# Kernel optimization log

Hardware: AMD Instinct MI355X
Metric: run time of the kernel (lower is better)

The kernel has to match this reference:

```python
import jax, jax.numpy as jnp
import numpy as np

E, NB, F, H = 30, 12, 1024, 32  # numEmotions, numBasicEmotions, numCommonFeatures, hidden
EPS = 1e-12  # F.normalize eps


def setup_inputs() -> dict:
    key = jax.random.key(0)
    ks = jax.random.split(key, 7)
    B, L = 8192, 128
    return {
        "basicEmotionDistributions": jax.random.uniform(ks[0], (B, NB, L), dtype=jnp.float32),
        "encodedFeatures": jax.random.normal(ks[1], (B, F), dtype=jnp.float32),
        "allBasicEmotionWeights": jax.random.normal(ks[2], (E, 1, NB, 1), dtype=jnp.float32),
        "W1": jax.random.normal(ks[3], (E, F, H), dtype=jnp.float32) / np.sqrt(F),
        "b1": jax.random.normal(ks[4], (E, H), dtype=jnp.float32) * 0.01,
        "W2": jax.random.normal(ks[5], (E, H, NB), dtype=jnp.float32) / np.sqrt(H),
        "b2": jax.random.normal(ks[6], (E, NB), dtype=jnp.float32) * 0.01,
    }


def reference(basicEmotionDistributions, encodedFeatures, allBasicEmotionWeights, W1, b1, W2, b2):
    # L1-normalize exp(weights) along basic-emotion dim: (E, NB)
    ew = jnp.exp(allBasicEmotionWeights[:, 0, :, 0])  # (E, NB)
    allW = ew / jnp.maximum(jnp.sum(jnp.abs(ew), axis=1, keepdims=True), EPS)

    # Batched per-emotion 2-layer MLP: (E, B, NB)
    h = jax.nn.selu(jnp.einsum('bf,efh->ebh', encodedFeatures, W1) + b1[:, None, :])
    mlp = jnp.einsum('ebh,ehn->ebn', h, W2) + b2[:, None, :]

    # updated weights and signed L1 normalization over NB dim
    updated = allW[:, None, :] + mlp  # (E, B, NB)
    # sign(x) * normalize(|x|, p=1) == x / max(sum|x|, eps)
    w = updated / jnp.maximum(jnp.sum(jnp.abs(updated), axis=2, keepdims=True), EPS)

    # weighted sum over basic emotions, then softmax over emotion length
    mixed = jnp.einsum('ebn,bnl->ebl', w, basicEmotionDistributions)  # (E, B, L)
    return jax.nn.softmax(mixed, axis=2)
```

## Files before the change

kernel.cpp:

```cpp
#include <hip/hip_runtime.h>

typedef __attribute__((ext_vector_type(8))) _Float16 half8;
typedef __attribute__((ext_vector_type(4))) float f32x4;

#define GAS(p) ((const __attribute__((address_space(1))) void*)(p))
#define LAS(p) ((__attribute__((address_space(3))) void*)(p))

__global__ __launch_bounds__(256) void cvt_pre(const float* __restrict__ feat,
                                               const float* __restrict__ W1,
                                               _Float16* __restrict__ A16,
                                               _Float16* __restrict__ W1T) {
    if (blockIdx.x < 4096) {
        int gid = blockIdx.x * 256 + threadIdx.x;
        int k8   = gid & 3;
        int m    = (gid >> 2) & 15;
        int frag = gid >> 6;
        int mf = frag & 7;
        int kc = (frag >> 3) & 31;
        int bt = frag >> 8;
        int b  = bt * 128 + mf * 16 + m;
        int f0 = kc * 32 + k8 * 8;
        const float4* src = (const float4*)(feat + (size_t)b * 1024 + f0);
        float4 v0 = src[0], v1 = src[1];
        half8 o;
        o[0] = (_Float16)v0.x; o[1] = (_Float16)v0.y;
        o[2] = (_Float16)v0.z; o[3] = (_Float16)v0.w;
        o[4] = (_Float16)v1.x; o[5] = (_Float16)v1.y;
        o[6] = (_Float16)v1.z; o[7] = (_Float16)v1.w;
        *(half8*)(A16 + ((size_t)frag * 64 + k8 * 16 + m) * 8) = o;
    } else {
        int gid = (blockIdx.x - 4096) * 256 + threadIdx.x;
        int k8   = gid & 3;
        int n    = (gid >> 2) & 15;
        int frag = gid >> 6;
        int nf = frag & 1;
        int kc = (frag >> 1) & 31;
        int e  = frag >> 6;
        int h  = nf * 16 + n;
        int f0 = kc * 32 + k8 * 8;
        const float* src = W1 + ((size_t)e * 1024 + f0) * 32 + h;
        half8 o;
#pragma unroll
        for (int j = 0; j < 8; ++j) o[j] = (_Float16)src[j * 32];
        *(half8*)(W1T + ((size_t)frag * 64 + k8 * 16 + n) * 8) = o;
    }
}

__global__ __launch_bounds__(256) void gemm_mlp(
    const _Float16* __restrict__ A16, const _Float16* __restrict__ W1T,
    const float* __restrict__ b1, const float* __restrict__ W2,
    const float* __restrict__ b2, const float* __restrict__ wts,
    float* __restrict__ wbuf) {
    __shared__ __align__(16) unsigned char smem[28672];
    unsigned char* Ash = smem;
    unsigned char* Bsh = smem + 16384;
    float* w2s = (float*)(smem + 24576);
    float* cb2 = (float*)(smem + 27648);
    float* ews = cb2 + 24;
    float* h_sh = (float*)smem;

    const int tid = threadIdx.x;
    const int e0 = blockIdx.x * 2;
    const int bt = blockIdx.y;
    const int w  = tid >> 6, l = tid & 63;
    const int q  = l >> 4, lc = l & 15;

    for (int i = tid; i < 768; i += 256) w2s[i] = W2[e0 * 384 + i];
    if (tid < 24) {
        cb2[tid] = b2[e0 * 12 + tid];
        ews[tid] = __expf(wts[e0 * 12 + tid]);
    }

    const _Float16* Abase = A16 + (size_t)bt * 131072;
    const _Float16* Bbase = W1T + (size_t)e0 * 32768;

    f32x4 zero = {0.f, 0.f, 0.f, 0.f};
    f32x4 acc[2][4];
#pragma unroll
    for (int i = 0; i < 2; ++i)
#pragma unroll
        for (int j = 0; j < 4; ++j) acc[i][j] = zero;

    for (int it = 0; it < 16; ++it) {
        const _Float16* Ait = Abase + it * 8192;
#pragma unroll
        for (int i = 0; i < 4; ++i) {
            int s = w * 4 + i;
            __builtin_amdgcn_global_load_lds(GAS(Ait + s * 512 + l * 8),
                                             LAS(Ash + s * 1024), 16, 0, 0);
        }
#pragma unroll
        for (int j = 0; j < 2; ++j) {
            int f  = w * 2 + j;
            int be = f >> 2, kn = f & 3;
            __builtin_amdgcn_global_load_lds(
                GAS(Bbase + be * 32768 + it * 2048 + kn * 512 + l * 8),
                LAS(Bsh + f * 1024), 16, 0, 0);
        }
        __syncthreads();
#pragma unroll
        for (int kc2 = 0; kc2 < 2; ++kc2) {
            half8 a0  = *(half8*)(Ash + (kc2 * 8 + 2 * w + 0) * 1024 + l * 16);
            half8 a1  = *(half8*)(Ash + (kc2 * 8 + 2 * w + 1) * 1024 + l * 16);
            half8 b00 = *(half8*)(Bsh + (0 + kc2 * 2 + 0) * 1024 + l * 16);
            half8 b01 = *(half8*)(Bsh + (0 + kc2 * 2 + 1) * 1024 + l * 16);
            half8 b10 = *(half8*)(Bsh + (4 + kc2 * 2 + 0) * 1024 + l * 16);
            half8 b11 = *(half8*)(Bsh + (4 + kc2 * 2 + 1) * 1024 + l * 16);
            acc[0][0] = __builtin_amdgcn_mfma_f32_16x16x32_f16(a0, b00, acc[0][0], 0, 0, 0);
            acc[0][1] = __builtin_amdgcn_mfma_f32_16x16x32_f16(a0, b01, acc[0][1], 0, 0, 0);
            acc[0][2] = __builtin_amdgcn_mfma_f32_16x16x32_f16(a0, b10, acc[0][2], 0, 0, 0);
            acc[0][3] = __builtin_amdgcn_mfma_f32_16x16x32_f16(a0, b11, acc[0][3], 0, 0, 0);
            acc[1][0] = __builtin_amdgcn_mfma_f32_16x16x32_f16(a1, b00, acc[1][0], 0, 0, 0);
            acc[1][1] = __builtin_amdgcn_mfma_f32_16x16x32_f16(a1, b01, acc[1][1], 0, 0, 0);
            acc[1][2] = __builtin_amdgcn_mfma_f32_16x16x32_f16(a1, b10, acc[1][2], 0, 0, 0);
            acc[1][3] = __builtin_amdgcn_mfma_f32_16x16x32_f16(a1, b11, acc[1][3], 0, 0, 0);
        }
        __syncthreads();
    }

    const float SC = 1.0507009873554805f, AL = 1.6732632423543772f;
    const int m2 = tid >> 1, sub = tid & 1;

#pragma unroll
    for (int eo = 0; eo < 2; ++eo) {
        const float b1a = b1[(e0 + eo) * 32 + lc];
        const float b1b = b1[(e0 + eo) * 32 + 16 + lc];
#pragma unroll
        for (int mf = 0; mf < 2; ++mf)
#pragma unroll
            for (int nf = 0; nf < 2; ++nf)
#pragma unroll
                for (int r = 0; r < 4; ++r) {
                    int m   = w * 32 + mf * 16 + q * 4 + r;
                    int col = nf * 16 + lc;
                    float x = acc[mf][eo * 2 + nf][r] + (nf ? b1b : b1a);
                    float hv = x > 0.f ? SC * x : SC * AL * (__expf(x) - 1.f);
                    h_sh[m * 33 + col] = hv;
                }
        __syncthreads();

        float u[6] = {0.f, 0.f, 0.f, 0.f, 0.f, 0.f};
        const float* hrow = h_sh + m2 * 33;
        const float* wbase = w2s + eo * 384 + sub * 6;
#pragma unroll 8
        for (int h = 0; h < 32; ++h) {
            float hv = hrow[h];
            const float* wr = wbase + h * 12;
#pragma unroll
            for (int j = 0; j < 6; ++j) u[j] += hv * wr[j];
        }
        float sew = 0.f;
#pragma unroll
        for (int i = 0; i < 12; ++i) sew += ews[eo * 12 + i];
        sew = fmaxf(sew, 1e-12f);
        float sabs = 0.f;
#pragma unroll
        for (int j = 0; j < 6; ++j) {
            u[j] += cb2[eo * 12 + sub * 6 + j] + ews[eo * 12 + sub * 6 + j] / sew;
            sabs += fabsf(u[j]);
        }
        sabs += __shfl_xor(sabs, 1);
        float inv = 1.f / fmaxf(sabs, 1e-12f);
        int b = bt * 128 + m2;
        float* dst = wbuf + (size_t)(e0 + eo) * 98304 + b * 12 + sub * 6;
#pragma unroll
        for (int j = 0; j < 6; ++j) dst[j] = u[j] * inv;
        __syncthreads();
    }
}

__global__ __launch_bounds__(256) void mix_softmax(
    const float* __restrict__ dist, const float* __restrict__ wbuf,
    float* __restrict__ out) {
    __shared__ float wsm[8 * 360];
    const int tid = threadIdx.x;
    const int b0 = blockIdx.x * 8;
    for (int i = tid; i < 2880; i += 256) {
        int e = i / 96, r = i - e * 96;
        wsm[(r / 12) * 360 + e * 12 + (r % 12)] = wbuf[(size_t)e * 98304 + b0 * 12 + r];
    }
    __syncthreads();
    const int m = tid >> 5, l4 = tid & 31;
    const int b = b0 + m;
    const float* dbase = dist + (size_t)b * 1536 + l4 * 4;
    f32x4 d[12];
#pragma unroll
    for (int n = 0; n < 12; ++n) d[n] = *(const f32x4*)(dbase + n * 128);
    const float* wrow = wsm + m * 360;
    for (int e = 0; e < 30; ++e) {
        const float* wr = wrow + e * 12;
        f32x4 a = {0.f, 0.f, 0.f, 0.f};
#pragma unroll
        for (int n = 0; n < 12; ++n) a += wr[n] * d[n];
        f32x4 ex;
        ex[0] = __expf(a[0]); ex[1] = __expf(a[1]);
        ex[2] = __expf(a[2]); ex[3] = __expf(a[3]);
        float sm = ex[0] + ex[1] + ex[2] + ex[3];
#pragma unroll
        for (int s = 16; s >= 1; s >>= 1) sm += __shfl_xor(sm, s);
        f32x4 o = ex * (1.f / sm);
        *(f32x4*)(out + ((size_t)e * 8192 + b) * 128 + l4 * 4) = o;
    }
}

extern "C" void kernel_launch(void* const* d_in, const int* in_sizes, int n_in,
                              void* d_out, int out_size, void* d_ws, size_t ws_size,
                              hipStream_t stream) {
    const float* dist = (const float*)d_in[0];
    const float* feat = (const float*)d_in[1];
    const float* wts  = (const float*)d_in[2];
    const float* W1   = (const float*)d_in[3];
    const float* b1   = (const float*)d_in[4];
    const float* W2   = (const float*)d_in[5];
    const float* b2   = (const float*)d_in[6];
    float* out = (float*)d_out;

    _Float16* A16 = (_Float16*)d_ws;
    _Float16* W1T = (_Float16*)((char*)d_ws + 16777216);
    float*   wbuf = (float*)((char*)d_ws + 16777216 + 1966080);

    cvt_pre<<<4576, 256, 0, stream>>>(feat, W1, A16, W1T);
    dim3 g1(15, 64);
    gemm_mlp<<<g1, 256, 0, stream>>>(A16, W1T, b1, W2, b2, wts, wbuf);
    mix_softmax<<<1024, 256, 0, stream>>>(dist, wbuf, out);
}
```

Baseline: 251.3 us.

## Process three emotions per GEMM block with swizzled 1D grid and repacked W2

```diff
diff --git a/kernel.cpp b/kernel.cpp
--- a/kernel.cpp
+++ b/kernel.cpp
@@ -51,22 +51,29 @@
     const float* __restrict__ b1, const float* __restrict__ W2,
     const float* __restrict__ b2, const float* __restrict__ wts,
     float* __restrict__ wbuf) {
-    __shared__ __align__(16) unsigned char smem[28672];
+    __shared__ __align__(16) unsigned char smem[33600];
     unsigned char* Ash = smem;
     unsigned char* Bsh = smem + 16384;
-    float* w2s = (float*)(smem + 24576);
-    float* cb2 = (float*)(smem + 27648);
-    float* ews = cb2 + 24;
+    float* w2s = (float*)(smem + 28672);
+    float* cb2 = (float*)(smem + 33280);
+    float* ews = cb2 + 36;
     float* h_sh = (float*)smem;
 
     const int tid = threadIdx.x;
-    const int e0 = blockIdx.x * 2;
-    const int bt = blockIdx.y;
+    const int bid = blockIdx.x;
+    const int v   = bid >> 3;
+    const int bt  = ((bid & 7) << 3) | (v & 7);
+    const int e0  = (v >> 3) * 3;
     const int w  = tid >> 6, l = tid & 63;
     const int q  = l >> 4, lc = l & 15;
 
-    for (int i = tid; i < 768; i += 256) w2s[i] = W2[e0 * 384 + i];
-    if (tid < 24) {
+    for (int i = tid; i < 1152; i += 256) {
+        int eo = i / 384, rr = i - eo * 384;
+        int h  = rr / 12, n = rr - h * 12;
+        int sb = n / 6,  j = n - sb * 6;
+        w2s[eo * 384 + sb * 192 + h * 6 + j] = W2[e0 * 384 + i];
+    }
+    if (tid < 36) {
         cb2[tid] = b2[e0 * 12 + tid];
         ews[tid] = __expf(wts[e0 * 12 + tid]);
     }
@@ -75,11 +82,11 @@
     const _Float16* Bbase = W1T + (size_t)e0 * 32768;
 
     f32x4 zero = {0.f, 0.f, 0.f, 0.f};
-    f32x4 acc[2][4];
+    f32x4 acc[2][6];
 #pragma unroll
     for (int i = 0; i < 2; ++i)
 #pragma unroll
-        for (int j = 0; j < 4; ++j) acc[i][j] = zero;
+        for (int j = 0; j < 6; ++j) acc[i][j] = zero;
 
     for (int it = 0; it < 16; ++it) {
         const _Float16* Ait = Abase + it * 8192;
@@ -90,8 +97,8 @@
                                              LAS(Ash + s * 1024), 16, 0, 0);
         }
 #pragma unroll
-        for (int j = 0; j < 2; ++j) {
-            int f  = w * 2 + j;
+        for (int j = 0; j < 3; ++j) {
+            int f  = w * 3 + j;
             int be = f >> 2, kn = f & 3;
             __builtin_amdgcn_global_load_lds(
                 GAS(Bbase + be * 32768 + it * 2048 + kn * 512 + l * 8),
@@ -100,20 +107,21 @@
         __syncthreads();
 #pragma unroll
         for (int kc2 = 0; kc2 < 2; ++kc2) {
-            half8 a0  = *(half8*)(Ash + (kc2 * 8 + 2 * w + 0) * 1024 + l * 16);
-            half8 a1  = *(half8*)(Ash + (kc2 * 8 + 2 * w + 1) * 1024 + l * 16);
-            half8 b00 = *(half8*)(Bsh + (0 + kc2 * 2 + 0) * 1024 + l * 16);
-            half8 b01 = *(half8*)(Bsh + (0 + kc2 * 2 + 1) * 1024 + l * 16);
-            half8 b10 = *(half8*)(Bsh + (4 + kc2 * 2 + 0) * 1024 + l * 16);
-            half8 b11 = *(half8*)(Bsh + (4 + kc2 * 2 + 1) * 1024 + l * 16);
-            acc[0][0] = __builtin_amdgcn_mfma_f32_16x16x32_f16(a0, b00, acc[0][0], 0, 0, 0);
-            acc[0][1] = __builtin_amdgcn_mfma_f32_16x16x32_f16(a0, b01, acc[0][1], 0, 0, 0);
-            acc[0][2] = __builtin_amdgcn_mfma_f32_16x16x32_f16(a0, b10, acc[0][2], 0, 0, 0);
-            acc[0][3] = __builtin_amdgcn_mfma_f32_16x16x32_f16(a0, b11, acc[0][3], 0, 0, 0);
-            acc[1][0] = __builtin_amdgcn_mfma_f32_16x16x32_f16(a1, b00, acc[1][0], 0, 0, 0);
-            acc[1][1] = __builtin_amdgcn_mfma_f32_16x16x32_f16(a1, b01, acc[1][1], 0, 0, 0);
-            acc[1][2] = __builtin_amdgcn_mfma_f32_16x16x32_f16(a1, b10, acc[1][2], 0, 0, 0);
-            acc[1][3] = __builtin_amdgcn_mfma_f32_16x16x32_f16(a1, b11, acc[1][3], 0, 0, 0);
+            half8 a0 = *(half8*)(Ash + (kc2 * 8 + 2 * w + 0) * 1024 + l * 16);
+            half8 a1 = *(half8*)(Ash + (kc2 * 8 + 2 * w + 1) * 1024 + l * 16);
+            half8 bfr[6];
+#pragma unroll
+            for (int be = 0; be < 3; ++be)
+#pragma unroll
+                for (int nf = 0; nf < 2; ++nf)
+                    bfr[be * 2 + nf] =
+                        *(half8*)(Bsh + (be * 4 + kc2 * 2 + nf) * 1024 + l * 16);
+#pragma unroll
+            for (int j = 0; j < 6; ++j)
+                acc[0][j] = __builtin_amdgcn_mfma_f32_16x16x32_f16(a0, bfr[j], acc[0][j], 0, 0, 0);
+#pragma unroll
+            for (int j = 0; j < 6; ++j)
+                acc[1][j] = __builtin_amdgcn_mfma_f32_16x16x32_f16(a1, bfr[j], acc[1][j], 0, 0, 0);
         }
         __syncthreads();
     }
@@ -122,7 +130,7 @@
     const int m2 = tid >> 1, sub = tid & 1;
 
 #pragma unroll
-    for (int eo = 0; eo < 2; ++eo) {
+    for (int eo = 0; eo < 3; ++eo) {
         const float b1a = b1[(e0 + eo) * 32 + lc];
         const float b1b = b1[(e0 + eo) * 32 + 16 + lc];
 #pragma unroll
@@ -135,19 +143,21 @@
                     int col = nf * 16 + lc;
                     float x = acc[mf][eo * 2 + nf][r] + (nf ? b1b : b1a);
                     float hv = x > 0.f ? SC * x : SC * AL * (__expf(x) - 1.f);
-                    h_sh[m * 33 + col] = hv;
+                    h_sh[m * 34 + col] = hv;
                 }
         __syncthreads();
 
         float u[6] = {0.f, 0.f, 0.f, 0.f, 0.f, 0.f};
-        const float* hrow = h_sh + m2 * 33;
-        const float* wbase = w2s + eo * 384 + sub * 6;
-#pragma unroll 8
-        for (int h = 0; h < 32; ++h) {
-            float hv = hrow[h];
-            const float* wr = wbase + h * 12;
-#pragma unroll
-            for (int j = 0; j < 6; ++j) u[j] += hv * wr[j];
+        const float2* hrow = (const float2*)(h_sh + m2 * 34);
+        const float* wbase = w2s + eo * 384 + sub * 192;
+#pragma unroll
+        for (int hp = 0; hp < 16; ++hp) {
+            float2 hv = hrow[hp];
+            const float* w0 = wbase + hp * 12;
+#pragma unroll
+            for (int j = 0; j < 6; ++j) u[j] += hv.x * w0[j];
+#pragma unroll
+            for (int j = 0; j < 6; ++j) u[j] += hv.y * w0[6 + j];
         }
         float sew = 0.f;
 #pragma unroll
@@ -220,7 +230,6 @@
     float*   wbuf = (float*)((char*)d_ws + 16777216 + 1966080);
 
     cvt_pre<<<4576, 256, 0, stream>>>(feat, W1, A16, W1T);
-    dim3 g1(15, 64);
-    gemm_mlp<<<g1, 256, 0, stream>>>(A16, W1T, b1, W2, b2, wts, wbuf);
+    gemm_mlp<<<640, 256, 0, stream>>>(A16, W1T, b1, W2, b2, wts, wbuf);
     mix_softmax<<<1024, 256, 0, stream>>>(dist, wbuf, out);
 }
```

New measurement: 263.0 us. +4.7%, slower.
